# Performance work log

Hardware: AMD Instinct MI355X
Metric: run time of the kernel (lower is better)

The kernel has to match this reference:

```python
import jax, jax.numpy as jnp
import numpy as np

B, NZ, ND, SDIM, H = 16384, 64, 8, 128, 512


def setup_inputs() -> dict:
    key = jax.random.key(0)
    ks = jax.random.split(key, 20)
    n = lambda i, shape, scale=0.02: (jax.random.normal(ks[i], shape, jnp.float32) * scale)
    return {
        "z": jax.random.normal(ks[0], (B, NZ), jnp.float32),
        "y": jax.random.randint(ks[1], (B,), 0, ND),
        # shared MLP: nz->512, 512->512 x3, ReLU after each
        "W0": n(2, (NZ, H)), "b0": jnp.zeros((H,), jnp.float32),
        "W1": n(3, (H, H)),  "b1": jnp.zeros((H,), jnp.float32),
        "W2": n(4, (H, H)),  "b2": jnp.zeros((H,), jnp.float32),
        "W3": n(5, (H, H)),  "b3": jnp.zeros((H,), jnp.float32),
        "U1": n(6, (ND, H, H)), "c1": jnp.zeros((ND, 1, H), jnp.float32),
        "U2": n(7, (ND, H, H)), "c2": jnp.zeros((ND, 1, H), jnp.float32),
        "U3": n(8, (ND, H, H)), "c3": jnp.zeros((ND, 1, H), jnp.float32),
        "Uo": n(9, (ND, H, SDIM)), "co": jnp.zeros((ND, 1, SDIM), jnp.float32),
    }


def reference(z, y, W0, b0, W1, b1, W2, b2, W3, b3, U1, c1, U2, c2, U3, c3, Uo, co):
    # shared trunk: [B, nz] -> [B, 512]
    h = jax.nn.relu(z @ W0 + b0)
    h = jax.nn.relu(h @ W1 + b1)
    h = jax.nn.relu(h @ W2 + b2)
    h = jax.nn.relu(h @ W3 + b3)
    # densely compute all nd unshared branches (faithful to torch stack-then-index)
    s = jax.nn.relu(jnp.einsum('bh,dhk->dbk', h, U1) + c1)   # [nd, B, 512]
    s = jax.nn.relu(jnp.einsum('dbh,dhk->dbk', s, U2) + c2)
    s = jax.nn.relu(jnp.einsum('dbh,dhk->dbk', s, U3) + c3)
    s = jnp.einsum('dbh,dhk->dbk', s, Uo) + co               # [nd, B, sdim]
    # gather-select the branch indexed by each sample's domain label y
    return s[y, jnp.arange(z.shape[0])]                      # [B, sdim]
```

## Files before the change

kernel.cpp:

```cpp
#include <hip/hip_runtime.h>

#define B_    16384
#define NZ_   64
#define ND_   8
#define SDIM_ 128
#define H_    512
#define CAP_  2320
#define NTB_  29

typedef _Float16 f16;
typedef __attribute__((ext_vector_type(4))) _Float16 half4;
typedef __attribute__((ext_vector_type(8))) _Float16 half8;
typedef __attribute__((ext_vector_type(4))) float floatx4;

__device__ __forceinline__ int pswz_t(int row, int colbyte) {
    return (row * 1024 + colbyte) ^ (((row >> 1) & 7) << 4);
}
__device__ __forceinline__ int pswz_b(int row, int colbyte) {
    return (row * 1024 + colbyte) ^ ((row & 7) << 4);
}

__device__ __forceinline__ void tr_mat(float (*tb)[33], const float* __restrict__ s,
                                       f16* __restrict__ dd, int K, int N, int tl) {
    const int ntk = K >> 5;
    const int per = ntk * (N >> 5);
    const int bt  = tl / per;
    const int w   = tl - bt * per;
    s  += (size_t)bt * K * N;
    dd += (size_t)bt * K * N;
    const int k0 = (w % ntk) << 5, n0 = (w / ntk) << 5;
    const int tid = threadIdx.x;
    {
        const int nn = tid & 31, k4 = tid >> 5;
        #pragma unroll
        for (int p = 0; p < 4; p++)
            tb[k4 + p * 8][nn] = s[(size_t)(k0 + k4 + p * 8) * N + n0 + nn];
    }
    __syncthreads();
    {
        const int sub = tid >> 7, r = tid & 127;
        const int lane = r >> 1, jp = (r & 1) * 4;
        const int kb = lane >> 4, l15 = lane & 15;
        const size_t base = ((size_t)((n0 >> 4) + sub) * (K >> 5) + (k0 >> 5)) * 512
                          + lane * 8 + jp;
        half4 h;
        #pragma unroll
        for (int jj = 0; jj < 4; jj++)
            h[jj] = (f16)tb[kb * 8 + jp + jj][sub * 16 + l15];
        *(half4*)(dd + base) = h;
    }
}

__global__ __launch_bounds__(256) void tr_k(
    const float* W0, const float* W1, const float* W2, const float* W3,
    const float* U1, const float* U2, const float* U3, const float* Uo,
    f16* W0t, f16* W1t, f16* W2t, f16* W3t,
    f16* U1t, f16* U2t, f16* U3t, f16* Uot)
{
    __shared__ float tb[32][33];
    int tl = blockIdx.x;
    if (tl < 32)   { tr_mat(tb, W0, W0t, 64, 512, tl); return; }  tl -= 32;
    if (tl < 256)  { tr_mat(tb, W1, W1t, 512, 512, tl); return; } tl -= 256;
    if (tl < 256)  { tr_mat(tb, W2, W2t, 512, 512, tl); return; } tl -= 256;
    if (tl < 256)  { tr_mat(tb, W3, W3t, 512, 512, tl); return; } tl -= 256;
    if (tl < 2048) { tr_mat(tb, U1, U1t, 512, 512, tl); return; } tl -= 2048;
    if (tl < 2048) { tr_mat(tb, U2, U2t, 512, 512, tl); return; } tl -= 2048;
    if (tl < 2048) { tr_mat(tb, U3, U3t, 512, 512, tl); return; } tl -= 2048;
    tr_mat(tb, Uo, Uot, 512, 128, tl);
}
#define TR_BLOCKS 7456

__global__ __launch_bounds__(256) void sort_k(const int* __restrict__ y,
                                              int* __restrict__ cnt,
                                              int* __restrict__ rowmap) {
    __shared__ int h[ND_], base[ND_];
    if (threadIdx.x < ND_) h[threadIdx.x] = 0;
    __syncthreads();
    const int b = blockIdx.x * 256 + threadIdx.x;
    const int d = y[b];
    const int r = atomicAdd(&h[d], 1);
    __syncthreads();
    if (threadIdx.x < ND_) base[threadIdx.x] = atomicAdd(&cnt[threadIdx.x], h[threadIdx.x]);
    __syncthreads();
    rowmap[d * CAP_ + base[d] + r] = b;
}

template<int MFRAG, int NFRAG, int KT, int NFN, int KTN, int SB, bool RELU, bool TOPANEL>
__device__ __forceinline__ void layer_t(
    char* lds, const half8* __restrict__ wp, const half8* __restrict__ wpn,
    const float* __restrict__ bias, half8 (&b)[3][4])
{
    const int t = threadIdx.x;
    const int lane = t & 63, wid = t >> 6;
    const int l15 = lane & 15, kb = lane >> 4;

    int baseA[MFRAG];
    #pragma unroll
    for (int m = 0; m < MFRAG; m++)
        baseA[m] = (((m * 16 + l15) * 1024) + kb * 16) ^ (((l15 >> 1) & 7) << 4);

    half8 a[2][MFRAG];
    #pragma unroll
    for (int m = 0; m < MFRAG; m++) a[0][m] = *(const half8*)(lds + baseA[m]);

    floatx4 acc[MFRAG][NFRAG] = {};

    #pragma unroll
    for (int kt = 0; kt < KT; kt++) {
        const int cur = kt & 1;
        if (kt + 1 < KT) {
            #pragma unroll
            for (int m = 0; m < MFRAG; m++)
                a[cur ^ 1][m] = *(const half8*)(lds + (baseA[m] ^ ((kt + 1) << 6)));
        }
        if (kt + 2 < KT) {
            #pragma unroll
            for (int n = 0; n < NFRAG; n++)
                b[(SB + kt + 2) % 3][n] = wp[((wid * NFRAG + n) * KT + kt + 2) * 64 + lane];
        } else if constexpr (NFN > 0) {
            const int s2 = kt + 2 - KT;
            #pragma unroll
            for (int n = 0; n < NFN; n++)
                b[(SB + kt + 2) % 3][n] = wpn[((wid * NFN + n) * KTN + s2) * 64 + lane];
        }
        __builtin_amdgcn_s_setprio(1);
        #pragma unroll
        for (int m = 0; m < MFRAG; m++)
            #pragma unroll
            for (int n = 0; n < NFRAG; n++)
                acc[m][n] = __builtin_amdgcn_mfma_f32_16x16x32_f16(
                    a[cur][m], b[(SB + kt) % 3][n], acc[m][n], 0, 0, 0);
        __builtin_amdgcn_s_setprio(0);
    }

    __syncthreads();

    #pragma unroll
    for (int n = 0; n < NFRAG; n++) {
        const int col = wid * (NFRAG * 16) + n * 16 + l15;
        const float bb = bias[col];
        #pragma unroll
        for (int m = 0; m < MFRAG; m++) {
            #pragma unroll
            for (int e = 0; e < 4; e++) {
                const int row = m * 16 + kb * 4 + e;
                float v = acc[m][n][e] + bb;
                if constexpr (RELU) v = fmaxf(v, 0.0f);
                *(f16*)(lds + pswz_t(row, col * 2)) = (f16)v;
            }
        }
    }
    __syncthreads();
}

__global__ __launch_bounds__(512, 2) void trunk_k(
    const float* __restrict__ z,
    const f16* __restrict__ W0p, const float* __restrict__ b0,
    const f16* __restrict__ W1p, const float* __restrict__ b1,
    const f16* __restrict__ W2p, const float* __restrict__ b2,
    const f16* __restrict__ W3p, const float* __restrict__ b3,
    f16* __restrict__ hT)
{
    extern __shared__ char lds[];
    const int t = threadIdx.x;
    const int row0 = blockIdx.x * 64;
    const int lane = t & 63, wid = t >> 6;

    const half8* w0 = (const half8*)W0p;
    const half8* w1 = (const half8*)W1p;
    const half8* w2 = (const half8*)W2p;
    const half8* w3 = (const half8*)W3p;

    half8 b[3][4];
    #pragma unroll
    for (int s = 0; s < 2; s++)
        #pragma unroll
        for (int n = 0; n < 4; n++)
            b[s][n] = w0[((wid * 4 + n) * 2 + s) * 64 + lane];

    {
        const int r = t >> 3, c = (t & 7) * 8;
        const float4 v0 = *(const float4*)(z + (size_t)(row0 + r) * NZ_ + c);
        const float4 v1 = *(const float4*)(z + (size_t)(row0 + r) * NZ_ + c + 4);
        half8 h = { (f16)v0.x, (f16)v0.y, (f16)v0.z, (f16)v0.w,
                    (f16)v1.x, (f16)v1.y, (f16)v1.z, (f16)v1.w };
        *(half8*)(lds + pswz_t(r, c * 2)) = h;
    }
    __syncthreads();

    layer_t<4, 4, 2,  4, 16, 0, true, true>(lds, w0, w1, b0, b);
    layer_t<4, 4, 16, 4, 16, 2, true, true>(lds, w1, w2, b1, b);
    layer_t<4, 4, 16, 4, 16, 0, true, true>(lds, w2, w3, b2, b);
    layer_t<4, 4, 16, 0, 16, 1, true, true>(lds, w3, w3, b3, b);

    {
        const int r = t >> 3;
        #pragma unroll
        for (int p = 0; p < 8; p++) {
            const int c16 = (t & 7) + p * 8;
            half8 h = *(const half8*)(lds + pswz_t(r, c16 * 16));
            *(half8*)(hT + (size_t)(row0 + r) * H_ + c16 * 8) = h;
        }
    }
}

template<int MFRAG, int NFRAG, int KT, bool RELU, bool TOPANEL>
__device__ __forceinline__ void layer_b(
    char* lds, const half8* __restrict__ wp, const float* __restrict__ bias,
    float* __restrict__ outf, const int* __restrict__ rmt, int vend)
{
    const int t = threadIdx.x;
    const int lane = t & 63, wid = t >> 6;
    const int l15 = lane & 15, kb = lane >> 4;
    const int swz = (l15 & 7) << 4;

    int baseA[MFRAG];
    #pragma unroll
    for (int m = 0; m < MFRAG; m++)
        baseA[m] = (((m * 16 + l15) * 1024) + kb * 16) ^ swz;

    int idxB[NFRAG];
    #pragma unroll
    for (int n = 0; n < NFRAG; n++)
        idxB[n] = ((wid * NFRAG + n) * KT) * 64 + lane;

    floatx4 acc[MFRAG][NFRAG] = {};
    half8 a[2][MFRAG], b[2][NFRAG];

    #pragma unroll
    for (int m = 0; m < MFRAG; m++) a[0][m] = *(const half8*)(lds + baseA[m]);
    #pragma unroll
    for (int n = 0; n < NFRAG; n++) b[0][n] = wp[idxB[n]];

    #pragma unroll
    for (int kt = 0; kt < KT; kt++) {
        const int cur = kt & 1, nxt = cur ^ 1;
        if (kt + 1 < KT) {
            #pragma unroll
            for (int m = 0; m < MFRAG; m++)
                a[nxt][m] = *(const half8*)(lds + (baseA[m] ^ ((kt + 1) << 6)));
            #pragma unroll
            for (int n = 0; n < NFRAG; n++)
                b[nxt][n] = wp[idxB[n] + (kt + 1) * 64];
        }
        #pragma unroll
        for (int m = 0; m < MFRAG; m++)
            #pragma unroll
            for (int n = 0; n < NFRAG; n++)
                acc[m][n] = __builtin_amdgcn_mfma_f32_16x16x32_f16(
                    a[cur][m], b[cur][n], acc[m][n], 0, 0, 0);
    }

    __syncthreads();

    #pragma unroll
    for (int n = 0; n < NFRAG; n++) {
        const int col = wid * (NFRAG * 16) + n * 16 + l15;
        const float bb = bias[col];
        #pragma unroll
        for (int m = 0; m < MFRAG; m++) {
            #pragma unroll
            for (int e = 0; e < 4; e++) {
                const int row = m * 16 + kb * 4 + e;
                float v = acc[m][n][e] + bb;
                if constexpr (RELU) v = fmaxf(v, 0.0f);
                if constexpr (TOPANEL) {
                    *(f16*)(lds + pswz_b(row, col * 2)) = (f16)v;
                } else {
                    if (row < vend) outf[(size_t)rmt[row] * SDIM_ + col] = v;
                }
            }
        }
    }
    if constexpr (TOPANEL) __syncthreads();
}

__global__ __launch_bounds__(512, 2) void branch_k(
    const f16* __restrict__ hT,
    const f16* __restrict__ U1p, const float* __restrict__ c1,
    const f16* __restrict__ U2p, const float* __restrict__ c2,
    const f16* __restrict__ U3p, const float* __restrict__ c3,
    const f16* __restrict__ Uop, const float* __restrict__ co,
    const int* __restrict__ cnt, const int* __restrict__ rowmap,
    float* __restrict__ out)
{
    extern __shared__ char lds[];
    const int d = blockIdx.x & 7, i = blockIdx.x >> 3;
    const int c = cnt[d];
    if (i * 80 >= c) return;
    const int vend = c - i * 80;
    const int* rmt = rowmap + d * CAP_ + i * 80;
    const int t = threadIdx.x;

    #pragma unroll
    for (int p = 0; p < 10; p++) {
        const int r   = p * 8 + (t >> 6);
        const int c16 = t & 63;
        const int src = rmt[r];
        half8 h = *(const half8*)(hT + (size_t)src * H_ + c16 * 8);
        *(half8*)(lds + pswz_b(r, c16 * 16)) = h;
    }
    __syncthreads();

    const half8* u1 = (const half8*)(U1p + (size_t)d * H_ * H_);
    const half8* u2 = (const half8*)(U2p + (size_t)d * H_ * H_);
    const half8* u3 = (const half8*)(U3p + (size_t)d * H_ * H_);
    const half8* uo = (const half8*)(Uop + (size_t)d * H_ * SDIM_);

    layer_b<5, 4, 16, true,  true >(lds, u1, c1 + d * H_,    nullptr, nullptr, 0);
    layer_b<5, 4, 16, true,  true >(lds, u2, c2 + d * H_,    nullptr, nullptr, 0);
    layer_b<5, 4, 16, true,  true >(lds, u3, c3 + d * H_,    nullptr, nullptr, 0);
    layer_b<5, 1, 16, false, false>(lds, uo, co + d * SDIM_, out, rmt, vend);
}

extern "C" void kernel_launch(void* const* d_in, const int* in_sizes, int n_in,
                              void* d_out, int out_size, void* d_ws, size_t ws_size,
                              hipStream_t stream)
{
    const float* z  = (const float*)d_in[0];
    const int*   y  = (const int*)d_in[1];
    const float* W0 = (const float*)d_in[2];
    const float* b0 = (const float*)d_in[3];
    const float* W1 = (const float*)d_in[4];
    const float* b1 = (const float*)d_in[5];
    const float* W2 = (const float*)d_in[6];
    const float* b2 = (const float*)d_in[7];
    const float* W3 = (const float*)d_in[8];
    const float* b3 = (const float*)d_in[9];
    const float* U1 = (const float*)d_in[10];
    const float* c1 = (const float*)d_in[11];
    const float* U2 = (const float*)d_in[12];
    const float* c2 = (const float*)d_in[13];
    const float* U3 = (const float*)d_in[14];
    const float* c3 = (const float*)d_in[15];
    const float* Uo = (const float*)d_in[16];
    const float* co = (const float*)d_in[17];
    float* out = (float*)d_out;

    char* p = (char*)d_ws;
    auto take = [&](size_t nbytes) { char* r = p; p += (nbytes + 255) & ~(size_t)255; return r; };
    int* cnt    = (int*)take(ND_ * 4);
    int* rowmap = (int*)take((size_t)ND_ * CAP_ * 4);
    f16* W0t = (f16*)take((size_t)H_ * NZ_ * 2);
    f16* W1t = (f16*)take((size_t)H_ * H_ * 2);
    f16* W2t = (f16*)take((size_t)H_ * H_ * 2);
    f16* W3t = (f16*)take((size_t)H_ * H_ * 2);
    f16* U1t = (f16*)take((size_t)ND_ * H_ * H_ * 2);
    f16* U2t = (f16*)take((size_t)ND_ * H_ * H_ * 2);
    f16* U3t = (f16*)take((size_t)ND_ * H_ * H_ * 2);
    f16* Uot = (f16*)take((size_t)ND_ * SDIM_ * H_ * 2);
    f16* hT  = (f16*)take((size_t)B_ * H_ * 2);

    hipFuncSetAttribute((const void*)trunk_k,  hipFuncAttributeMaxDynamicSharedMemorySize, 64 * 1024);
    hipFuncSetAttribute((const void*)branch_k, hipFuncAttributeMaxDynamicSharedMemorySize, 80 * 1024);

    hipMemsetAsync(cnt, 0, ND_ * 4, stream);
    hipMemsetAsync(rowmap, 0, (size_t)ND_ * CAP_ * 4, stream);
    sort_k<<<dim3(B_ / 256), dim3(256), 0, stream>>>(y, cnt, rowmap);

    tr_k<<<dim3(TR_BLOCKS), dim3(256), 0, stream>>>(W0, W1, W2, W3, U1, U2, U3, Uo,
                                                    W0t, W1t, W2t, W3t, U1t, U2t, U3t, Uot);

    trunk_k<<<dim3(B_ / 64), dim3(512), 64 * 1024, stream>>>(
        z, W0t, b0, W1t, b1, W2t, b2, W3t, b3, hT);

    branch_k<<<dim3(8 * NTB_), dim3(512), 80 * 1024, stream>>>(
        hT, U1t, c1, U2t, c2, U3t, c3, Uot, co, cnt, rowmap, out);
}
```

Before: 98.70 us.

## Stage branch weights through LDS with async global-to-LDS double buffering

The branch-layer GEMM now streams weight fragments into a double-buffered LDS region with global_load_lds and explicit vmcnt waits, instead of loading them directly from global memory into registers. MFMA issue is wrapped in raised wave priority so loads for stage k+2 overlap compute on stage k. This grows branch_k's LDS to 144 KB and lowers launch bounds to one block per CU, trading occupancy for deeper explicit prefetch. The hand-placed waitcnt sequencing is fragile if the compiler reorders memory operations.

```diff
diff --git a/kernel.cpp b/kernel.cpp
--- a/kernel.cpp
+++ b/kernel.cpp
@@ -12,6 +12,18 @@
 typedef __attribute__((ext_vector_type(4))) _Float16 half4;
 typedef __attribute__((ext_vector_type(8))) _Float16 half8;
 typedef __attribute__((ext_vector_type(4))) float floatx4;
+
+#define VMCNT4 asm volatile("s_waitcnt vmcnt(4)" ::: "memory")
+#define VMCNT1 asm volatile("s_waitcnt vmcnt(1)" ::: "memory")
+#define VMCNT0 asm volatile("s_waitcnt vmcnt(0)" ::: "memory")
+#define LGKM0  asm volatile("s_waitcnt lgkmcnt(0)" ::: "memory")
+
+__device__ __forceinline__ void gload16(const void* gp, void* lp) {
+    void* g = const_cast<void*>(gp);
+    __builtin_amdgcn_global_load_lds(
+        (__attribute__((address_space(1))) void*)g,
+        (__attribute__((address_space(3))) void*)lp, 16, 0, 0);
+}
 
 __device__ __forceinline__ int pswz_t(int row, int colbyte) {
     return (row * 1024 + colbyte) ^ (((row >> 1) & 7) << 4);
@@ -205,50 +217,68 @@
 }
 
 template<int MFRAG, int NFRAG, int KT, bool RELU, bool TOPANEL>
-__device__ __forceinline__ void layer_b(
-    char* lds, const half8* __restrict__ wp, const float* __restrict__ bias,
+__device__ __forceinline__ void layer_c(
+    char* lds, char* ldsB, const f16* __restrict__ Wp, const float* __restrict__ bias,
     float* __restrict__ outf, const int* __restrict__ rmt, int vend)
 {
     const int t = threadIdx.x;
     const int lane = t & 63, wid = t >> 6;
     const int l15 = lane & 15, kb = lane >> 4;
     const int swz = (l15 & 7) << 4;
+    constexpr int BUFSZ = 8 * NFRAG * 1024;
 
     int baseA[MFRAG];
     #pragma unroll
     for (int m = 0; m < MFRAG; m++)
         baseA[m] = (((m * 16 + l15) * 1024) + kb * 16) ^ swz;
 
-    int idxB[NFRAG];
-    #pragma unroll
-    for (int n = 0; n < NFRAG; n++)
-        idxB[n] = ((wid * NFRAG + n) * KT) * 64 + lane;
-
+    char* chunk = ldsB + wid * (NFRAG * 1024);
+    const f16* gw = Wp + (size_t)wid * NFRAG * KT * 512 + lane * 8;
+
+    auto stage = [&](int s) {
+        #pragma unroll
+        for (int n = 0; n < NFRAG; n++)
+            gload16(gw + ((size_t)n * KT + s) * 512,
+                    chunk + (s & 1) * BUFSZ + n * 1024);
+    };
+    auto readB = [&](int s, half8 (&br)[NFRAG]) {
+        #pragma unroll
+        for (int n = 0; n < NFRAG; n++)
+            br[n] = *(const half8*)(chunk + (s & 1) * BUFSZ + n * 1024 + lane * 16);
+    };
+
+    half8 a[2][MFRAG], br[2][NFRAG];
     floatx4 acc[MFRAG][NFRAG] = {};
-    half8 a[2][MFRAG], b[2][NFRAG];
-
+
+    stage(0); stage(1);
+    if constexpr (NFRAG == 4) VMCNT4; else VMCNT1;
+    readB(0, br[0]);
     #pragma unroll
     for (int m = 0; m < MFRAG; m++) a[0][m] = *(const half8*)(lds + baseA[m]);
-    #pragma unroll
-    for (int n = 0; n < NFRAG; n++) b[0][n] = wp[idxB[n]];
 
     #pragma unroll
     for (int kt = 0; kt < KT; kt++) {
         const int cur = kt & 1, nxt = cur ^ 1;
+        __builtin_amdgcn_s_setprio(1);
+        #pragma unroll
+        for (int m = 0; m < MFRAG; m++)
+            #pragma unroll
+            for (int n = 0; n < NFRAG; n++)
+                acc[m][n] = __builtin_amdgcn_mfma_f32_16x16x32_f16(
+                    a[cur][m], br[cur][n], acc[m][n], 0, 0, 0);
+        __builtin_amdgcn_s_setprio(0);
+        if (kt + 2 < KT) {
+            LGKM0;
+            stage(kt + 2);
+        }
         if (kt + 1 < KT) {
+            if (kt + 2 < KT) { if constexpr (NFRAG == 4) VMCNT4; else VMCNT1; }
+            else             { VMCNT0; }
+            readB(kt + 1, br[nxt]);
             #pragma unroll
             for (int m = 0; m < MFRAG; m++)
                 a[nxt][m] = *(const half8*)(lds + (baseA[m] ^ ((kt + 1) << 6)));
-            #pragma unroll
-            for (int n = 0; n < NFRAG; n++)
-                b[nxt][n] = wp[idxB[n] + (kt + 1) * 64];
-        }
-        #pragma unroll
-        for (int m = 0; m < MFRAG; m++)
-            #pragma unroll
-            for (int n = 0; n < NFRAG; n++)
-                acc[m][n] = __builtin_amdgcn_mfma_f32_16x16x32_f16(
-                    a[cur][m], b[cur][n], acc[m][n], 0, 0, 0);
+        }
     }
 
     __syncthreads();
@@ -275,7 +305,7 @@
     if constexpr (TOPANEL) __syncthreads();
 }
 
-__global__ __launch_bounds__(512, 2) void branch_k(
+__global__ __launch_bounds__(512, 1) void branch_k(
     const f16* __restrict__ hT,
     const f16* __restrict__ U1p, const float* __restrict__ c1,
     const f16* __restrict__ U2p, const float* __restrict__ c2,
@@ -285,6 +315,7 @@
     float* __restrict__ out)
 {
     extern __shared__ char lds[];
+    char* ldsB = lds + 80 * 1024;
     const int d = blockIdx.x & 7, i = blockIdx.x >> 3;
     const int c = cnt[d];
     if (i * 80 >= c) return;
@@ -302,15 +333,15 @@
     }
     __syncthreads();
 
-    const half8* u1 = (const half8*)(U1p + (size_t)d * H_ * H_);
-    const half8* u2 = (const half8*)(U2p + (size_t)d * H_ * H_);
-    const half8* u3 = (const half8*)(U3p + (size_t)d * H_ * H_);
-    const half8* uo = (const half8*)(Uop + (size_t)d * H_ * SDIM_);
-
-    layer_b<5, 4, 16, true,  true >(lds, u1, c1 + d * H_,    nullptr, nullptr, 0);
-    layer_b<5, 4, 16, true,  true >(lds, u2, c2 + d * H_,    nullptr, nullptr, 0);
-    layer_b<5, 4, 16, true,  true >(lds, u3, c3 + d * H_,    nullptr, nullptr, 0);
-    layer_b<5, 1, 16, false, false>(lds, uo, co + d * SDIM_, out, rmt, vend);
+    const f16* u1 = U1p + (size_t)d * H_ * H_;
+    const f16* u2 = U2p + (size_t)d * H_ * H_;
+    const f16* u3 = U3p + (size_t)d * H_ * H_;
+    const f16* uo = Uop + (size_t)d * H_ * SDIM_;
+
+    layer_c<5, 4, 16, true,  true >(lds, ldsB, u1, c1 + d * H_,    nullptr, nullptr, 0);
+    layer_c<5, 4, 16, true,  true >(lds, ldsB, u2, c2 + d * H_,    nullptr, nullptr, 0);
+    layer_c<5, 4, 16, true,  true >(lds, ldsB, u3, c3 + d * H_,    nullptr, nullptr, 0);
+    layer_c<5, 1, 16, false, false>(lds, ldsB, uo, co + d * SDIM_, out, rmt, vend);
 }
 
 extern "C" void kernel_launch(void* const* d_in, const int* in_sizes, int n_in,
@@ -352,7 +383,7 @@
     f16* hT  = (f16*)take((size_t)B_ * H_ * 2);
 
     hipFuncSetAttribute((const void*)trunk_k,  hipFuncAttributeMaxDynamicSharedMemorySize, 64 * 1024);
-    hipFuncSetAttribute((const void*)branch_k, hipFuncAttributeMaxDynamicSharedMemorySize, 80 * 1024);
+    hipFuncSetAttribute((const void*)branch_k, hipFuncAttributeMaxDynamicSharedMemorySize, 144 * 1024);
 
     hipMemsetAsync(cnt, 0, ND_ * 4, stream);
     hipMemsetAsync(rowmap, 0, (size_t)ND_ * CAP_ * 4, stream);
@@ -364,6 +395,6 @@
     trunk_k<<<dim3(B_ / 64), dim3(512), 64 * 1024, stream>>>(
         z, W0t, b0, W1t, b1, W2t, b2, W3t, b3, hT);
 
-    branch_k<<<dim3(8 * NTB_), dim3(512), 80 * 1024, stream>>>(
+    branch_k<<<dim3(8 * NTB_), dim3(512), 144 * 1024, stream>>>(
         hT, U1t, c1, U2t, c2, U3t, c3, Uot, co, cnt, rowmap, out);
 }
```

After: 89.64 us. 1.1x faster.
